# Kernel optimization log

Measured on AMD Instinct MI355X. Metric: run time of the kernel, lower is better.

Reference implementation:

```python
import jax, jax.numpy as jnp
import numpy as np
from jax import lax

B, T, C, H, W = 2, 5, 2, 128, 256
E, M, L = 64, 16, 4  # embedding_dim, n_fno_modes, n_fno_layers
EPS = 1e-5


def conv1x1(x, w, b):
    # x: [N, I, H, W], w: [O, I], b: [O]
    return jnp.einsum('nihw,oi->nohw', x, w) + b[None, :, None, None]


def conv3x3(x, w, b):
    # x: [N, I, H, W], w: [O, I, 3, 3]
    y = lax.conv_general_dilated(x, w, window_strides=(1, 1), padding='SAME',
                                 dimension_numbers=('NCHW', 'OIHW', 'NCHW'))
    return y + b[None, :, None, None]


def instance_norm(x):
    # InstanceNorm2d(affine=False): normalize over H,W per (n, c), biased var
    mu = jnp.mean(x, axis=(2, 3), keepdims=True)
    var = jnp.var(x, axis=(2, 3), keepdims=True)
    return (x - mu) * lax.rsqrt(var + EPS)


def upsample2x_nearest(x):
    return jnp.repeat(jnp.repeat(x, 2, axis=2), 2, axis=3)


def resize_nearest(x, out_h, out_w):
    # torch F.interpolate mode='nearest': idx = floor(i * in / out)
    in_h, in_w = x.shape[2], x.shape[3]
    hi = (jnp.arange(out_h) * in_h) // out_h
    wi = (jnp.arange(out_w) * in_w) // out_w
    return x[:, :, hi, :][:, :, :, wi]


def fno_layer(x, wr, wi, cw, cb):
    # x: [N, E, H, W]; wr/wi: [2, E, E, M, M]; cw: [E, E]; cb: [E]
    h, w = x.shape[2], x.shape[3]
    coeff = jnp.fft.rfft2(x, axes=(2, 3), norm='ortho')  # [N, E, H, W//2+1]
    w0 = wr[0] + 1j * wi[0]
    w1 = wr[1] + 1j * wi[1]
    out = jnp.zeros_like(coeff)
    out = out.at[:, :, :M, :M].set(
        jnp.einsum('nixy,ioxy->noxy', coeff[:, :, :M, :M], w0))
    out = out.at[:, :, -M:, :M].set(
        jnp.einsum('nixy,ioxy->noxy', coeff[:, :, -M:, :M], w1))
    spec = jnp.fft.irfft2(out, s=(h, w), axes=(2, 3), norm='ortho')
    return jax.nn.gelu(conv1x1(x, cw, cb) + spec, approximate=False)


def setup_inputs() -> dict:
    key = jax.random.key(0)
    ks = jax.random.split(key, 10)
    s = 0.02
    return {
        'sensor_value': jax.random.normal(ks[0], (B, T, C, H, W), jnp.float32),
        'updim_w': 0.3 * jax.random.normal(ks[1], (E, C), jnp.float32),
        'updim_b': jnp.zeros((E,), jnp.float32),
        'smooth_w': 0.04 * jax.random.normal(ks[2], (E, E, 3, 3), jnp.float32),
        'smooth_b': jnp.zeros((E,), jnp.float32),
        'fno_wr': s * jax.random.normal(ks[3], (L, 2, E, E, M, M), jnp.float32),
        'fno_wi': s * jax.random.normal(ks[4], (L, 2, E, E, M, M), jnp.float32),
        'fno_cw': 0.1 * jax.random.normal(ks[5], (L, E, E), jnp.float32),
        'fno_cb': jnp.zeros((L, E), jnp.float32),
        'downdim_w': 0.1 * jax.random.normal(ks[6], (C, E), jnp.float32),
        'downdim_b': jnp.zeros((C,), jnp.float32),
    }


def reference(sensor_value, updim_w, updim_b, smooth_w, smooth_b,
              fno_wr, fno_wi, fno_cw, fno_cb, downdim_w, downdim_b):
    b, t, c, h, w = sensor_value.shape
    x = sensor_value.reshape(b * t, c, h, w)
    x = conv1x1(x, updim_w, updim_b)
    x = upsample2x_nearest(x)
    x = jax.nn.gelu(instance_norm(conv3x3(x, smooth_w, smooth_b)), approximate=False)
    x = resize_nearest(x, H, W)
    for l in range(L):
        x = fno_layer(x, fno_wr[l], fno_wi[l], fno_cw[l], fno_cb[l])
    x = conv1x1(x, downdim_w, downdim_b)
    return x.reshape(b, t, c, H, W)
```

## Files before the change

### kernel.cpp

```cpp
#include <hip/hip_runtime.h>
#include <math.h>

#define PI_D 3.14159265358979323846


typedef _Float16 h8 __attribute__((ext_vector_type(8)));
typedef float f16v __attribute__((ext_vector_type(16)));

__device__ __forceinline__ float gelu_f(float v){
  return 0.5f*v*(1.0f + erff(v*0.70710678118654752440f));
}

__global__ __launch_bounds__(256) void k_tables(float* __restrict__ twFwH, float* __restrict__ twBwH,
                                                _Float16* __restrict__ Tspec, _Float16* __restrict__ TdftW){
  int id = blockIdx.x*256 + threadIdx.x;
  if (id < 4096){
    int h = id >> 5, m = id & 31;
    int xm = (m < 16) ? m : (96 + m);
    double ang = -2.0*PI_D*(double)((xm*h) & 127)/128.0;
    twFwH[id*2]   = (float)cos(ang);
    twFwH[id*2+1] = (float)sin(ang);
  } else if (id < 8192){
    int j = id - 4096;
    int h = j >> 5, m = j & 31;
    int xm = (m < 16) ? m : (96 + m);
    double ang = 2.0*PI_D*(double)((xm*h) & 127)/128.0;
    twBwH[j*2]   = (float)cos(ang);
    twBwH[j*2+1] = (float)sin(ang);
  } else if (id < 16384){
    int j = id - 8192;
    int w = j >> 5, kk = j & 31;
    int y = kk >> 1;
    double ang = 2.0*PI_D*(double)((w*y) & 255)/256.0;
    double v = (kk & 1) ? -sin(ang) : cos(ang);
    Tspec[j] = (_Float16)v;
  } else if (id < 24576){
    int j = id - 16384;
    int y2 = j >> 8, w = j & 255;
    int y = y2 >> 1;
    double ang = -2.0*PI_D*(double)((w*y) & 255)/256.0;
    double v = (y2 & 1) ? sin(ang) : cos(ang);
    TdftW[j] = (_Float16)v;
  }
}

__global__ __launch_bounds__(256) void k_foldK(const float* __restrict__ smw, const float* __restrict__ upw,
                                               const float* __restrict__ upb, float* __restrict__ Keff){
  int id = blockIdx.x*256 + threadIdx.x;
  if (id >= 1024) return;
  int o = id >> 4, rs = (id >> 2) & 3, tap = id & 3;
  int r = rs >> 1, s = rs & 1, a = tap >> 1, b = tap & 1;
  int klo = (r==0) ? (a==0?0:1) : (a==0?0:2);
  int khi = (r==0) ? (a==0?0:2) : (a==0?1:2);
  int llo = (s==0) ? (b==0?0:1) : (b==0?0:2);
  int lhi = (s==0) ? (b==0?0:2) : (b==0?1:2);
  float a0=0.f, a1=0.f, ab=0.f;
  for (int i=0;i<64;++i){
    float t = 0.f;
    for (int kh=klo; kh<=khi; ++kh)
      for (int kw=llo; kw<=lhi; ++kw)
        t += smw[((size_t)o*64+i)*9 + kh*3+kw];
    a0 += t*upw[i*2];
    a1 += t*upw[i*2+1];
    ab += t*upb[i];
  }
  *(float4*)(Keff + o*64 + (rs*4+tap)*4) = make_float4(a0, a1, ab, 0.f);
}

__global__ __launch_bounds__(256) void k_transW(const float* __restrict__ wr, const float* __restrict__ wi,
                                                unsigned* __restrict__ Wt){
  __shared__ unsigned P[64*257];
  int lb = blockIdx.x;
  int i = lb & 63, blk = (lb>>6)&1, l = lb>>7;
  int tid = threadIdx.x;
  size_t sbase = (size_t)l*2097152 + (size_t)blk*1048576 + (size_t)i*16384 + tid;
  for (int o=0;o<64;++o){
    float a = wr[sbase + (size_t)o*256];
    float b = wi[sbase + (size_t)o*256];
    union { unsigned u; _Float16 h[2]; } pk;
    pk.h[0] = (_Float16)a; pk.h[1] = (_Float16)b;
    P[o*257 + tid] = pk.u;
  }
  __syncthreads();
  int o = tid & 63, g = tid >> 6;
  size_t dbase = (size_t)(l*2+blk)*1048576;
  for (int it=0; it<64; ++it){
    int my = g*64 + it;
    Wt[dbase + (size_t)my*4096 + i*64 + o] = P[o*257 + my];
  }
}

__global__ __launch_bounds__(512) void k_corr(const float* __restrict__ sv, float* __restrict__ Rpart){
  __shared__ float S[2][6][260];
  int bid = blockIdx.x;
  int band = bid & 31, n = bid >> 5;
  int u0 = band*4;
  int tid = threadIdx.x;
  for (int t = tid; t < 3120; t += 512){
    int ch = t / 1560; int rem = t - ch*1560; int rr = rem / 260; int ci = rem - rr*260;
    int row = u0 - 1 + rr, col = ci - 1;
    float v = 0.f;
    if (row >= 0 && row < 128 && col >= 0 && col < 256)
      v = sv[((size_t)(n*2+ch)*128 + row)*256 + col];
    S[ch][rr][ci] = v;
  }
  __syncthreads();

  int lane = tid & 63, wv = tid >> 6;
  int c  = (wv<4) ? (wv>>1) : ((wv<6) ? (wv-4) : 2);
  int c2 = (wv<4) ? (wv&1)  : ((wv<6) ? 2 : (wv-6));
  float acc[9];
  #pragma unroll
  for (int k=0;k<9;++k) acc[k]=0.f;

  for (int r=0;r<4;++r){
    int u = u0 + r, lu = r + 1;
    for (int cb=0;cb<4;++cb){
      int v = cb*64 + lane;
      float f = (c==2) ? 1.f : S[c][lu][1+v];
      #pragma unroll
      for (int dr=-1;dr<=1;++dr){
        int ur = u + dr;
        float rko = (ur>=0 && ur<128) ? 1.f : 0.f;
        #pragma unroll
        for (int dc=-1;dc<=1;++dc){
          float g;
          if (c2==2){
            int vc = v + dc;
            g = rko * ((vc>=0 && vc<256) ? 1.f : 0.f);
          } else {
            g = S[c2][lu+dr][1+v+dc];
          }
          acc[(dr+1)*3 + dc+1] += f*g;
        }
      }
    }
  }
  #pragma unroll
  for (int k=0;k<9;++k){
    float v = acc[k];
    for (int off=32; off; off>>=1) v += __shfl_xor(v, off);
    if (lane==0) Rpart[((size_t)(n*32+band)*8 + wv)*9 + k] = v;
  }
}

__global__ __launch_bounds__(256) void k_bnd(const float* __restrict__ sv, float* __restrict__ Bnd){
  __shared__ float E[4][3][260];
  int n = blockIdx.x, tid = threadIdx.x;
  for (int t = tid; t < 3120; t += 256){
    int e = t/780; int rem = t - e*780; int ch = rem/260; int i = rem - ch*260;
    int idx = i - 1;
    int len = (e<2) ? 256 : 128;
    float v = 0.f;
    if (idx >= 0 && idx < len){
      if (ch==2) v = 1.f;
      else {
        int row = (e==0) ? 0 : (e==1) ? 127 : idx;
        int col = (e==2) ? 0 : (e==3) ? 255 : idx;
        v = sv[((size_t)(n*2+ch)*128 + row)*256 + col];
      }
    }
    E[e][ch][i] = v;
  }
  __syncthreads();
  if (tid < 108){
    int e = tid/27; int rem = tid - e*27; int pair = rem/3; int lag = rem%3 - 1;
    int c = pair/3, c2 = pair%3;
    int len = (e<2) ? 256 : 128;
    float a = 0.f;
    for (int i=0;i<len;++i) a += E[e][c][1+i]*E[e][c2][1+i+lag];
    Bnd[n*144 + tid] = a;
  } else if (tid < 144){
    int t = tid - 108; int corner = t/9; int pair = t - corner*9;
    int c = pair/3, c2 = pair%3;
    int e = (corner<2) ? 0 : 1;
    int idx = (corner&1) ? 255 : 0;
    Bnd[n*144 + tid] = E[e][c][1+idx]*E[e][c2][1+idx];
  }
}

__global__ __launch_bounds__(256) void k_stats3(const float* __restrict__ Rpart, const float* __restrict__ Bnd,
                                                const float* __restrict__ Keff, float* __restrict__ stats){
  __shared__ float R[9][9];
  __shared__ float BL[4][9][3];
  __shared__ float CR[4][9];
  __shared__ float M[4][12][12];
  int n = blockIdx.x, tid = threadIdx.x;

  if (tid < 72){
    int wv = tid/9, k = tid - (tid/9)*9;
    double s = 0.0;
    for (int b=0;b<32;++b) s += (double)Rpart[((size_t)(n*32+b)*8 + wv)*9 + k];
    int c  = (wv<4) ? (wv>>1) : ((wv<6) ? (wv-4) : 2);
    int c2 = (wv<4) ? (wv&1)  : ((wv<6) ? 2 : (wv-6));
    R[c*3+c2][k] = (float)s;
  } else if (tid < 81){
    int k = tid - 72; int dr = k/3 - 1, dc = k%3 - 1;
    R[8][k] = (float)((128 - (dr<0?-dr:dr)) * (256 - (dc<0?-dc:dc)));
  }
  if (tid < 108){
    int e = tid/27, rem = tid - (tid/27)*27;
    BL[e][rem/3][rem%3] = Bnd[n*144 + tid];
  } else if (tid < 144){
    int t = tid - 108;
    CR[t/9][t - (t/9)*9] = Bnd[n*144 + tid];
  }
  __syncthreads();

  for (int t = tid; t < 576; t += 256){
    int rs = t/144; int rem = t - rs*144; int i = rem/12, j = rem - (rem/12)*12;
    int ab = i/3,  c  = i - ab*3,  a  = ab>>1, b  = ab&1;
    int ab2 = j/3, c2 = j - ab2*3, a2 = ab2>>1, b2 = ab2&1;
    int r = rs>>1, s = rs&1;
    int dr = a2 - a, dc = b2 - b;
    int pair = c*3 + c2;
    float g = R[pair][(dr+1)*3 + (dc+1)];
    if (r==1 && a==1 && a2==1) g -= BL[0][pair][dc+1];
    if (r==0 && a==0 && a2==0) g -= BL[1][pair][dc+1];
    if (s==1 && b==1 && b2==1) g -= BL[2][pair][dr+1];
    if (s==0 && b==0 && b2==0) g -= BL[3][pair][dr+1];
    bool rowc = (a==a2) && ((r==1 && a==1) || (r==0 && a==0));
    bool colc = (b==b2) && ((s==1 && b==1) || (s==0 && b==0));
    if (rowc && colc){
      int corner = ((r==1)?0:2) + ((s==1)?0:1);
      g += CR[corner][pair];
    }
    M[rs][i][j] = g;
  }
  __syncthreads();

  if (tid < 64){
    int o = tid;
    double S1 = 0.0, S2 = 0.0;
    for (int rs=0; rs<4; ++rs){
      float w[12];
      #pragma unroll
      for (int ab=0; ab<4; ++ab){
        float4 kv = *(const float4*)(Keff + o*64 + (rs*4+ab)*4);
        w[ab*3+0] = kv.x; w[ab*3+1] = kv.y; w[ab*3+2] = kv.z;
      }
      #pragma unroll
      for (int i=0;i<12;++i){
        double ti = 0.0;
        #pragma unroll
        for (int j=0;j<12;++j) ti += (double)M[rs][i][j]*(double)w[j];
        S2 += (double)w[i]*ti;
      }
      #pragma unroll
      for (int ab=0; ab<4; ++ab)
        #pragma unroll
        for (int c=0;c<3;++c)
          S1 += (double)w[ab*3+c]*(double)M[rs][ab*3+c][ab*3+2];
    }
    double mu  = S1 / 131072.0;
    double var = S2 / 131072.0 - mu*mu;
    stats[(n*64+o)*2]   = (float)mu;
    stats[(n*64+o)*2+1] = (float)(1.0/sqrt(var + 1e-5));
  }
}

__global__ __launch_bounds__(256) void k_convnorm(const float* __restrict__ sv,
                                                  const float* __restrict__ Keff,
                                                  const float* __restrict__ stats,
                                                  _Float16* __restrict__ act){
  __shared__ float SV[4*260];
  int bid = blockIdx.x;
  int p = bid & 127, n = bid >> 7;
  int tid = threadIdx.x;
  for (int t = tid; t < 1032; t += 256){
    int dr = t / 516;
    int rem = t - dr*516;
    int ch = rem / 258;
    int ci = rem - ch*258;
    int row = p - 1 + dr;
    int col = ci - 1;
    float v = 0.f;
    if (row >= 0 && col >= 0 && col < 256)
      v = sv[((size_t)(n*2+ch)*128 + row)*256 + col];
    SV[(dr*2+ch)*260 + ci] = v;
  }
  __syncthreads();

  int q = tid;
  float x0[4], x1[4], ib[4];
  float rowok0 = (p>0)?1.f:0.f;
  float colok0 = (q>0)?1.f:0.f;
  #pragma unroll
  for (int a=0;a<2;++a)
    #pragma unroll
    for (int b=0;b<2;++b){
      x0[a*2+b] = SV[(a*2+0)*260 + q + b];
      x1[a*2+b] = SV[(a*2+1)*260 + q + b];
      ib[a*2+b] = (a==0?rowok0:1.f) * (b==0?colok0:1.f);
    }

  for (int o=0; o<64; ++o){
    const float4* kp = (const float4*)(Keff + o*64);
    float y = 0.f;
    #pragma unroll
    for (int t=0;t<4;++t){
      float4 kv = kp[t];
      y += kv.x*x0[t] + kv.y*x1[t] + kv.z*ib[t];
    }
    float mu = stats[(n*64+o)*2], istd = stats[(n*64+o)*2+1];
    float v = (y - mu)*istd;
    act[((size_t)(n*64+o)*128 + p)*256 + q] = (_Float16)gelu_f(v);
  }
}

__global__ __launch_bounds__(256, 2) void k_dftW_mfma(const _Float16* __restrict__ act,
                                                      const _Float16* __restrict__ TdftW,
                                                      float* __restrict__ Cy){
  __shared__ _Float16 Ax[32768];
  __shared__ _Float16 Bt[8192];
  int tid = threadIdx.x;
  int hp = blockIdx.x & 63, n = blockIdx.x >> 6;
  int h0 = hp*2;

  {
    int a = tid >> 1;
    int ws = (tid & 1) * 128;
    int e = a & 63, ht = a >> 6;
    const _Float16* src = act + ((size_t)(n*64+e))*32768 + (size_t)(h0+ht)*256 + ws;
    #pragma unroll
    for (int k=0;k<16;++k){
      h8 v = *(const h8*)(src + k*8);
      int wq = (ws >> 3) + k;
      int chunk = wq ^ (a & 7);
      *(h8*)(Ax + a*256 + chunk*8) = v;
    }
  }
  {
    int y2 = tid & 31, ws = (tid >> 5) * 32;
    const _Float16* src = TdftW + y2*256 + ws;
    #pragma unroll
    for (int k=0;k<4;++k){
      h8 v = *(const h8*)(src + k*8);
      int wq = (ws >> 3) + k;
      int chunk = wq ^ (y2 & 7);
      *(h8*)(Bt + y2*256 + chunk*8) = v;
    }
  }
  __syncthreads();

  int lane = tid & 63;
  int l31 = lane & 31, l5 = lane >> 5;
  int mt = tid >> 6;
  int a = mt*32 + l31;

  f16v acc;
  #pragma unroll
  for (int j=0;j<16;++j) acc[j] = 0.f;
  #pragma unroll
  for (int ks=0;ks<16;++ks){
    int kb = ks*16 + l5*8;
    int cA = (kb>>3) ^ (a & 7);
    int cB = (kb>>3) ^ (l31 & 7);
    h8 af = *(const h8*)(Ax + a*256 + cA*8);
    h8 bf = *(const h8*)(Bt + l31*256 + cB*8);
    acc = __builtin_amdgcn_mfma_f32_32x32x16_f16(bf, af, acc, 0,0,0);
  }
  int e = a & 63, ht = a >> 6;
  #pragma unroll
  for (int j=0;j<16;j+=2){
    int y2 = (j&3) + 8*(j>>2) + 4*l5;
    int yy = y2 >> 1;
    *(float2*)(Cy + (((size_t)(n*16+yy)*128 + h0+ht)*64 + e)*2) = make_float2(acc[j], acc[j+1]);
  }
}

__global__ __launch_bounds__(256) void k_specAB(const float* __restrict__ Cy,
                                                const float* __restrict__ twF,
                                                const unsigned* __restrict__ Wt,
                                                float* __restrict__ MS, int l){
  __shared__ float CO[8*64*2];
  int bid = blockIdx.x;
  int mq = bid / 160;
  int pid = bid - mq*160;
  int y = pid & 15, n = pid >> 4;
  int tid = threadIdx.x;
  int lane = tid & 63;
  int wv = __builtin_amdgcn_readfirstlane(tid >> 6);

  {
    int m0 = mq*8 + wv*2;
    const float* cyb = Cy + (((size_t)(n*16+y)*128)*64 + lane)*2;
    const float* tf = twF + m0*2;
    float ar0=0.f, ai0=0.f, ar1=0.f, ai1=0.f;
    for (int h=0; h<128; ++h){
      float2 c = *(const float2*)(cyb + h*128);
      const float* tp = tf + h*64;
      float t0r = tp[0], t0i = tp[1], t1r = tp[2], t1i = tp[3];
      ar0 += t0r*c.x - t0i*c.y; ai0 += t0r*c.y + t0i*c.x;
      ar1 += t1r*c.x - t1i*c.y; ai1 += t1r*c.y + t1i*c.x;
    }
    int mm = wv*2;
    *(float2*)(CO + (mm*64 + lane)*2)     = make_float2(ar0, ai0);
    *(float2*)(CO + ((mm+1)*64 + lane)*2) = make_float2(ar1, ai1);
  }
  __syncthreads();

  {
    #pragma unroll
    for (int t2=0; t2<2; ++t2){
      int mm = wv*2 + t2;
      int m = mq*8 + mm;
      int blk = m >> 4, mloc = m & 15;
      int my = mloc*16 + y;
      const unsigned* wb = Wt + ((size_t)((l*2+blk)*256 + my))*4096 + lane;
      float mr = 0.f, mi = 0.f;
      for (int i=0;i<64;++i){
        float2 cc = *(const float2*)(CO + (mm*64 + i)*2);
        union { unsigned u; _Float16 h[2]; } pk;
        pk.u = wb[(size_t)i*64];
        float wr_f = (float)pk.h[0], wi_f = (float)pk.h[1];
        mr += cc.x*wr_f - cc.y*wi_f;
        mi += cc.x*wi_f + cc.y*wr_f;
      }
      *(float2*)(MS + (((size_t)(n*16+y)*32 + m)*64 + lane)*2) = make_float2(mr, mi);
    }
  }
}

__global__ __launch_bounds__(256) void k_specC(const float* __restrict__ MS,
                                               const float* __restrict__ twB,
                                               float* __restrict__ G){
  __shared__ float SM[32*64*2];
  int bid = blockIdx.x;
  int hq = bid / 160;
  int pid = bid - hq*160;
  int y = pid & 15, n = pid >> 4;
  int tid = threadIdx.x;
  int lane = tid & 63;
  int wv = __builtin_amdgcn_readfirstlane(tid >> 6);

  {
    const float4* src = (const float4*)(MS + ((size_t)(n*16+y)*32)*128);
    float4* dst = (float4*)SM;
    #pragma unroll
    for (int t=0; t<4; ++t) dst[tid + t*256] = src[tid + t*256];
  }
  __syncthreads();

  float f = (y==0) ? (1.f/32768.f) : (2.f/32768.f);
  for (int k=0;k<8;++k){
    int h = hq*32 + wv*8 + k;
    const float* tb = twB + h*64;
    float gr=0.f, gi=0.f;
    #pragma unroll
    for (int m=0;m<32;++m){
      float tr = tb[m*2], ti = tb[m*2+1];
      float2 mo2 = *(const float2*)(SM + (m*64+lane)*2);
      gr += tr*mo2.x - ti*mo2.y;
      gi += tr*mo2.y + ti*mo2.x;
    }
    size_t gb = (((size_t)(n*128+h)*16 + y)*2)*64 + lane;
    G[gb]      = gr*f;
    G[gb + 64] = gi*f;
  }
}

__global__ __launch_bounds__(256, 2) void k_combine_mfma(const _Float16* __restrict__ act_in,
                                                         const float* __restrict__ G,
                                                         const _Float16* __restrict__ Tspec,
                                                         const float* __restrict__ cw,
                                                         const float* __restrict__ cb,
                                                         _Float16* __restrict__ act_out){
  __shared__ _Float16 Bx[32768];
  __shared__ _Float16 At[8192];
  int tid = threadIdx.x;
  int h = blockIdx.x & 127, n = blockIdx.x >> 7;

  {
    int p = tid >> 3;
    int wl = tid & 7;
    int i0 = 2*p;
    const _Float16* r0 = act_in + (size_t)(n*64+i0)*32768 + (size_t)h*256;
    const _Float16* r1 = r0 + 32768;
    int cbase = (p >> 2);
    #pragma unroll
    for (int jj=0; jj<32; ++jj){
      int w = wl + 8*jj;
      union { _Float16 hh[2]; unsigned u; } pk;
      pk.hh[0] = r0[w]; pk.hh[1] = r1[w];
      int chunk = cbase ^ (w & 7);
      *(unsigned*)(Bx + w*128 + chunk*8 + (i0 & 7)) = pk.u;
    }
  }
  {
    int o = tid >> 2, seg = (tid & 3)*16;
    float4 c0 = *(const float4*)(cw + o*64 + seg);
    float4 c1 = *(const float4*)(cw + o*64 + seg + 4);
    float4 c2 = *(const float4*)(cw + o*64 + seg + 8);
    float4 c3 = *(const float4*)(cw + o*64 + seg + 12);
    h8 v0, v1;
    v0[0]=(_Float16)c0.x; v0[1]=(_Float16)c0.y; v0[2]=(_Float16)c0.z; v0[3]=(_Float16)c0.w;
    v0[4]=(_Float16)c1.x; v0[5]=(_Float16)c1.y; v0[6]=(_Float16)c1.z; v0[7]=(_Float16)c1.w;
    v1[0]=(_Float16)c2.x; v1[1]=(_Float16)c2.y; v1[2]=(_Float16)c2.z; v1[3]=(_Float16)c2.w;
    v1[4]=(_Float16)c3.x; v1[5]=(_Float16)c3.y; v1[6]=(_Float16)c3.z; v1[7]=(_Float16)c3.w;
    int cb0 = (seg>>3) ^ (o & 7);
    int cb1 = ((seg>>3)+1) ^ (o & 7);
    *(h8*)(At + o*128 + cb0*8) = v0;
    *(h8*)(At + o*128 + cb1*8) = v1;
  }
  {
    const float* gp = G + (size_t)(n*128 + h)*2048 + tid*8;
    float4 g0 = *(const float4*)gp;
    float4 g1 = *(const float4*)(gp + 4);
    float gv[8] = {g0.x,g0.y,g0.z,g0.w,g1.x,g1.y,g1.z,g1.w};
    int idx0 = tid*8;
    int yc = idx0 >> 6;
    int o0 = idx0 & 63;
    int kk = 64 + yc;
    #pragma unroll
    for (int j=0;j<8;++j){
      int o = o0 + j;
      int chunk = (kk >> 3) ^ (o & 7);
      At[o*128 + chunk*8 + (kk & 7)] = (_Float16)gv[j];
    }
  }
  {
    int w = tid;
    const _Float16* tp = Tspec + w*32;
    #pragma unroll
    for (int cc=0; cc<4; ++cc){
      h8 v = *(const h8*)(tp + cc*8);
      int chunk = (8 + cc) ^ (w & 7);
      *(h8*)(Bx + w*128 + chunk*8) = v;
    }
  }
  __syncthreads();

  int lane = tid & 63;
  int l31 = lane & 31, l5 = lane >> 5;
  int w0 = tid >> 6;
  int mt = w0 & 1, ng = w0 >> 1;
  int o_lane = mt*32 + l31;

  h8 af[6];
  #pragma unroll
  for (int ks=0;ks<6;++ks){
    int kb = ks*16 + l5*8;
    int chunk = (kb>>3) ^ (o_lane & 7);
    af[ks] = *(const h8*)(At + o_lane*128 + chunk*8);
  }
  float bias[16];
  #pragma unroll
  for (int j=0;j<16;++j) bias[j] = cb[mt*32 + (j&3) + 8*(j>>2) + 4*l5];

  f16v acc[4];
  #pragma unroll
  for (int q=0;q<4;++q)
    #pragma unroll
    for (int j=0;j<16;++j) acc[q][j] = bias[j];

  #pragma unroll
  for (int q=0;q<4;++q){
    int w = (ng*4+q)*32 + l31;
    const _Float16* bbase = Bx + w*128;
    int w7 = w & 7;
    #pragma unroll
    for (int ks=0;ks<6;++ks){
      int kb = ks*16 + l5*8;
      int chunk = (kb>>3) ^ w7;
      h8 bf = *(const h8*)(bbase + chunk*8);
      acc[q] = __builtin_amdgcn_mfma_f32_32x32x16_f16(af[ks], bf, acc[q], 0,0,0);
    }
  }

  #pragma unroll
  for (int q=0;q<4;++q){
    int wcol = (ng*4+q)*32 + l31;
    #pragma unroll
    for (int j=0;j<16;++j){
      int o = mt*32 + (j&3) + 8*(j>>2) + 4*l5;
      float v = gelu_f(acc[q][j]);
      act_out[(size_t)(n*64+o)*32768 + (size_t)h*256 + wcol] = (_Float16)v;
    }
  }
}

__global__ __launch_bounds__(256) void k_downdim(const _Float16* __restrict__ x, const float* __restrict__ wd,
                                                 const float* __restrict__ bd, float* __restrict__ out){
  size_t idx = (size_t)blockIdx.x*256 + threadIdx.x;
  int n = (int)(idx >> 15);
  int pos = (int)(idx & 32767);
  float a0 = bd[0], a1 = bd[1];
  const _Float16* xp = x + (size_t)n*2097152 + pos;
  for (int e=0;e<64;++e){
    float v = (float)xp[(size_t)e*32768];
    a0 += wd[e]*v;
    a1 += wd[64+e]*v;
  }
  out[(size_t)n*65536 + pos] = a0;
  out[(size_t)n*65536 + 32768 + pos] = a1;
}

extern "C" void kernel_launch(void* const* d_in, const int* in_sizes, int n_in,
                              void* d_out, int out_size, void* d_ws, size_t ws_size,
                              hipStream_t stream) {
  const float* sv  = (const float*)d_in[0];
  const float* upw = (const float*)d_in[1];
  const float* upb = (const float*)d_in[2];
  const float* smw = (const float*)d_in[3];
  const float* smb = (const float*)d_in[4];
  const float* fwr = (const float*)d_in[5];
  const float* fwi = (const float*)d_in[6];
  const float* fcw = (const float*)d_in[7];
  const float* fcb = (const float*)d_in[8];
  const float* ddw = (const float*)d_in[9];
  const float* ddb = (const float*)d_in[10];
  float* out = (float*)d_out;
  (void)smb;

  float* W = (float*)d_ws;
  _Float16* actA = (_Float16*)W;
  _Float16* actB = (_Float16*)(W + 10485760);
  float* Cy    = W + 20971520;
  float* G     = W + 23592960;
  float* part  = W + 26214400;
  float* stats = W + 28180480;
  float* Keff  = W + 28181760;
  float* twFwH = W + 28185856;
  float* twBwH = W + 28194048;
  _Float16* Tspec = (_Float16*)(W + 28202240);
  _Float16* TdftW = (_Float16*)(W + 28206336);
  unsigned* Wt   = (unsigned*)(W + 28210432);

  float* Rpart = part;
  float* Bnd   = part + 30000;
  float* MS    = part + 65536;

  k_tables<<<96,256,0,stream>>>(twFwH, twBwH, Tspec, TdftW);
  k_foldK<<<4,256,0,stream>>>(smw, upw, upb, Keff);
  k_transW<<<512,256,0,stream>>>(fwr, fwi, Wt);
  k_corr<<<320,512,0,stream>>>(sv, Rpart);
  k_bnd<<<10,256,0,stream>>>(sv, Bnd);
  k_stats3<<<10,256,0,stream>>>(Rpart, Bnd, Keff, stats);
  k_convnorm<<<1280,256,0,stream>>>(sv, Keff, stats, actA);

  _Float16* xa = actA; _Float16* xb = actB;
  for (int l=0;l<4;++l){
    k_dftW_mfma<<<640,256,0,stream>>>(xa, TdftW, Cy);
    k_specAB<<<640,256,0,stream>>>(Cy, twFwH, Wt, MS, l);
    k_specC<<<640,256,0,stream>>>(MS, twBwH, G);
    k_combine_mfma<<<1280,256,0,stream>>>(xa, G, Tspec, fcw + (size_t)l*4096, fcb + (size_t)l*64, xb);
    _Float16* t = xa; xa = xb; xb = t;
  }
  k_downdim<<<1280,256,0,stream>>>(xa, ddw, ddb, out);
}
```

Measured before the change: 524.0 us.

## Double combine kernel threads, vectorize activation staging, and re-swizzle LDS

```diff
diff --git a/kernel.cpp b/kernel.cpp
--- a/kernel.cpp
+++ b/kernel.cpp
@@ -10,6 +10,8 @@
 __device__ __forceinline__ float gelu_f(float v){
   return 0.5f*v*(1.0f + erff(v*0.70710678118654752440f));
 }
+
+__device__ __forceinline__ int fsw_c(int w){ return (w ^ (w >> 3)) & 7; }
 
 __global__ __launch_bounds__(256) void k_tables(float* __restrict__ twFwH, float* __restrict__ twBwH,
                                                 _Float16* __restrict__ Tspec, _Float16* __restrict__ TdftW){
@@ -460,7 +462,7 @@
   }
 }
 
-__global__ __launch_bounds__(256, 2) void k_combine_mfma(const _Float16* __restrict__ act_in,
+__global__ __launch_bounds__(512, 4) void k_combine_mfma(const _Float16* __restrict__ act_in,
                                                          const float* __restrict__ G,
                                                          const _Float16* __restrict__ Tspec,
                                                          const float* __restrict__ cw,
@@ -472,60 +474,58 @@
   int h = blockIdx.x & 127, n = blockIdx.x >> 7;
 
   {
-    int p = tid >> 3;
-    int wl = tid & 7;
-    int i0 = 2*p;
-    const _Float16* r0 = act_in + (size_t)(n*64+i0)*32768 + (size_t)h*256;
+    int rp = tid >> 4, sub = tid & 15;
+    int i0 = 2*rp;
+    int wbase = sub*16;
+    const _Float16* r0 = act_in + (size_t)(n*64+i0)*32768 + (size_t)h*256 + wbase;
     const _Float16* r1 = r0 + 32768;
-    int cbase = (p >> 2);
-    #pragma unroll
-    for (int jj=0; jj<32; ++jj){
-      int w = wl + 8*jj;
+    h8 A0 = *(const h8*)r0,     A1 = *(const h8*)(r0+8);
+    h8 B0 = *(const h8*)r1,     B1 = *(const h8*)(r1+8);
+    int cbs = rp >> 2;
+    int lo  = i0 & 7;
+    #pragma unroll
+    for (int k=0;k<16;++k){
       union { _Float16 hh[2]; unsigned u; } pk;
-      pk.hh[0] = r0[w]; pk.hh[1] = r1[w];
-      int chunk = cbase ^ (w & 7);
-      *(unsigned*)(Bx + w*128 + chunk*8 + (i0 & 7)) = pk.u;
-    }
-  }
-  {
-    int o = tid >> 2, seg = (tid & 3)*16;
+      pk.hh[0] = (k<8) ? A0[k] : A1[k-8];
+      pk.hh[1] = (k<8) ? B0[k] : B1[k-8];
+      int w = wbase + k;
+      int chunk = cbs ^ fsw_c(w);
+      *(unsigned*)(Bx + w*128 + chunk*8 + lo) = pk.u;
+    }
+  }
+  {
+    int o = tid >> 3, seg = (tid & 7)*8;
     float4 c0 = *(const float4*)(cw + o*64 + seg);
     float4 c1 = *(const float4*)(cw + o*64 + seg + 4);
-    float4 c2 = *(const float4*)(cw + o*64 + seg + 8);
-    float4 c3 = *(const float4*)(cw + o*64 + seg + 12);
-    h8 v0, v1;
-    v0[0]=(_Float16)c0.x; v0[1]=(_Float16)c0.y; v0[2]=(_Float16)c0.z; v0[3]=(_Float16)c0.w;
-    v0[4]=(_Float16)c1.x; v0[5]=(_Float16)c1.y; v0[6]=(_Float16)c1.z; v0[7]=(_Float16)c1.w;
-    v1[0]=(_Float16)c2.x; v1[1]=(_Float16)c2.y; v1[2]=(_Float16)c2.z; v1[3]=(_Float16)c2.w;
-    v1[4]=(_Float16)c3.x; v1[5]=(_Float16)c3.y; v1[6]=(_Float16)c3.z; v1[7]=(_Float16)c3.w;
-    int cb0 = (seg>>3) ^ (o & 7);
-    int cb1 = ((seg>>3)+1) ^ (o & 7);
-    *(h8*)(At + o*128 + cb0*8) = v0;
-    *(h8*)(At + o*128 + cb1*8) = v1;
-  }
-  {
-    const float* gp = G + (size_t)(n*128 + h)*2048 + tid*8;
-    float4 g0 = *(const float4*)gp;
-    float4 g1 = *(const float4*)(gp + 4);
-    float gv[8] = {g0.x,g0.y,g0.z,g0.w,g1.x,g1.y,g1.z,g1.w};
-    int idx0 = tid*8;
+    h8 v;
+    v[0]=(_Float16)c0.x; v[1]=(_Float16)c0.y; v[2]=(_Float16)c0.z; v[3]=(_Float16)c0.w;
+    v[4]=(_Float16)c1.x; v[5]=(_Float16)c1.y; v[6]=(_Float16)c1.z; v[7]=(_Float16)c1.w;
+    int ch0 = (seg>>3) ^ (o & 7);
+    *(h8*)(At + o*128 + ch0*8) = v;
+  }
+  {
+    const float* gp = G + (size_t)(n*128 + h)*2048 + tid*4;
+    float4 g = *(const float4*)gp;
+    float gv[4] = {g.x, g.y, g.z, g.w};
+    int idx0 = tid*4;
     int yc = idx0 >> 6;
     int o0 = idx0 & 63;
     int kk = 64 + yc;
     #pragma unroll
-    for (int j=0;j<8;++j){
+    for (int j=0;j<4;++j){
       int o = o0 + j;
       int chunk = (kk >> 3) ^ (o & 7);
       At[o*128 + chunk*8 + (kk & 7)] = (_Float16)gv[j];
     }
   }
   {
-    int w = tid;
-    const _Float16* tp = Tspec + w*32;
-    #pragma unroll
-    for (int cc=0; cc<4; ++cc){
-      h8 v = *(const h8*)(tp + cc*8);
-      int chunk = (8 + cc) ^ (w & 7);
+    int w = tid >> 1, half = tid & 1;
+    const _Float16* tp = Tspec + w*32 + half*16;
+    #pragma unroll
+    for (int c=0;c<2;++c){
+      h8 v = *(const h8*)(tp + c*8);
+      int cc = half*2 + c;
+      int chunk = (8 + cc) ^ fsw_c(w);
       *(h8*)(Bx + w*128 + chunk*8) = v;
     }
   }
@@ -533,8 +533,8 @@
 
   int lane = tid & 63;
   int l31 = lane & 31, l5 = lane >> 5;
-  int w0 = tid >> 6;
-  int mt = w0 & 1, ng = w0 >> 1;
+  int w0i = tid >> 6;
+  int mt = w0i & 1, ng = w0i >> 1;
   int o_lane = mt*32 + l31;
 
   h8 af[6];
@@ -548,29 +548,29 @@
   #pragma unroll
   for (int j=0;j<16;++j) bias[j] = cb[mt*32 + (j&3) + 8*(j>>2) + 4*l5];
 
-  f16v acc[4];
-  #pragma unroll
-  for (int q=0;q<4;++q)
+  f16v acc[2];
+  #pragma unroll
+  for (int q=0;q<2;++q)
     #pragma unroll
     for (int j=0;j<16;++j) acc[q][j] = bias[j];
 
   #pragma unroll
-  for (int q=0;q<4;++q){
-    int w = (ng*4+q)*32 + l31;
+  for (int q=0;q<2;++q){
+    int w = (ng*2+q)*32 + l31;
     const _Float16* bbase = Bx + w*128;
-    int w7 = w & 7;
+    int wf = fsw_c(w);
     #pragma unroll
     for (int ks=0;ks<6;++ks){
       int kb = ks*16 + l5*8;
-      int chunk = (kb>>3) ^ w7;
+      int chunk = (kb>>3) ^ wf;
       h8 bf = *(const h8*)(bbase + chunk*8);
       acc[q] = __builtin_amdgcn_mfma_f32_32x32x16_f16(af[ks], bf, acc[q], 0,0,0);
     }
   }
 
   #pragma unroll
-  for (int q=0;q<4;++q){
-    int wcol = (ng*4+q)*32 + l31;
+  for (int q=0;q<2;++q){
+    int wcol = (ng*2+q)*32 + l31;
     #pragma unroll
     for (int j=0;j<16;++j){
       int o = mt*32 + (j&3) + 8*(j>>2) + 4*l5;
@@ -644,7 +644,7 @@
     k_dftW_mfma<<<640,256,0,stream>>>(xa, TdftW, Cy);
     k_specAB<<<640,256,0,stream>>>(Cy, twFwH, Wt, MS, l);
     k_specC<<<640,256,0,stream>>>(MS, twBwH, G);
-    k_combine_mfma<<<1280,256,0,stream>>>(xa, G, Tspec, fcw + (size_t)l*4096, fcb + (size_t)l*64, xb);
+    k_combine_mfma<<<1280,512,0,stream>>>(xa, G, Tspec, fcw + (size_t)l*4096, fcb + (size_t)l*64, xb);
     _Float16* t = xa; xa = xb; xb = t;
   }
   k_downdim<<<1280,256,0,stream>>>(xa, ddw, ddb, out);
```

Result: faster. 493.9 us (-5.7%).
